# Optimization experiments

Measured on AMD Instinct MI355X. Metric: run time of the kernel, lower is better.

Reference implementation:

```python
import jax, jax.numpy as jnp
import numpy as np

B, T, D, H = 8, 1024, 512, 8
HD = D // H  # per-head hidden = embed_dim // n_head = 64
EPS = 1e-5


def setup_inputs() -> dict:
    key = jax.random.key(0)
    ks = jax.random.split(key, 8)
    x = jax.random.normal(ks[0], (B, T, D), dtype=jnp.float32)
    sc = 1.0 / np.sqrt(D)
    Wq = jax.random.normal(ks[1], (D, H * HD), dtype=jnp.float32) * sc
    Wk = jax.random.normal(ks[2], (D, H * HD), dtype=jnp.float32) * sc
    Wp = jax.random.normal(ks[3], (H * HD, D), dtype=jnp.float32) * sc
    bq = jnp.zeros((H * HD,), jnp.float32)
    bk = jnp.zeros((H * HD,), jnp.float32)
    bp = jnp.zeros((D,), jnp.float32)
    w_mlp = jax.random.normal(ks[4], (2 * HD,), dtype=jnp.float32) * 0.1
    ln_g = jnp.ones((D,), jnp.float32)
    ln_b = jnp.zeros((D,), jnp.float32)
    return {"x": x, "Wq": Wq, "bq": bq, "Wk": Wk, "bk": bk,
            "Wp": Wp, "bp": bp, "w_mlp": w_mlp, "ln_g": ln_g, "ln_b": ln_b}


def reference(x, Wq, bq, Wk, bk, Wp, bp, w_mlp, ln_g, ln_b):
    b, t, d = x.shape
    h, hd = H, HD
    # q/k projections, split into heads: [B,T,H,hd]
    qx = (x @ Wq + bq).reshape(b, t, h, hd)
    kx = (x @ Wk + bk).reshape(b, t, h, hd)
    # MLP score: tanh(concat(k_j, q_i) . w) == tanh(k_j.w[:hd] + q_i.w[hd:])
    k_s = jnp.einsum('bkhd,d->bkh', kx, w_mlp[:hd])   # [B,K,H]
    q_s = jnp.einsum('bqhd,d->bqh', qx, w_mlp[hd:])   # [B,Q,H]
    score = jnp.tanh(q_s[:, :, None, :] + k_s[:, None, :, :])  # [B,Q,K,H]
    attn = jax.nn.softmax(score, axis=2)  # softmax over k_len
    # values are the key projection kx (bmm(score, kx) in original)
    out = jnp.einsum('bqkh,bkhd->bqhd', attn, kx).reshape(b, t, h * hd)
    out = out @ Wp + bp  # output projection (dropout is identity at eval)
    # residual + LayerNorm
    y = x + out
    mu = jnp.mean(y, axis=-1, keepdims=True)
    var = jnp.var(y, axis=-1, keepdims=True)
    yn = (y - mu) * jax.lax.rsqrt(var + EPS)
    return yn * ln_g + ln_b
```

## Files before the change

kernel.cpp:

```cpp
#include <hip/hip_runtime.h>
#include <cstddef>

#define TT 1024
#define DDIM 512
#define HH 8
#define NND 128
#define NS 68

typedef __attribute__((ext_vector_type(8))) short bfrag;
typedef __attribute__((ext_vector_type(4))) float facc;

#define SC2   2.8853900817779268f
#define L2E   1.4426950408889634f

static __device__ __forceinline__ unsigned bfrne(float f) {
    unsigned u = __float_as_uint(f);
    return (u + 0x7fffu + ((u >> 16) & 1u)) >> 16;
}
static __device__ __forceinline__ unsigned pack2rne(float a, float b) {
    return bfrne(a) | (bfrne(b) << 16);
}
static __device__ __forceinline__ unsigned pack2hu(float a, float b) {
    return ((__float_as_uint(a) + 0x8000u) >> 16) |
           ((__float_as_uint(b) + 0x8000u) & 0xffff0000u);
}
static __device__ __forceinline__ void gl2lds16(const void* g, void* l) {
    __builtin_amdgcn_global_load_lds(
        (const __attribute__((address_space(1))) unsigned int*)g,
        (__attribute__((address_space(3))) unsigned int*)l, 16, 0, 0);
}
static __device__ __forceinline__ float wt(float t) {
    float r = __builtin_amdgcn_rcpf(t + 1.f);
    return __builtin_amdgcn_exp2f(fmaf(r, -2.f * L2E, L2E));
}

__global__ __launch_bounds__(256) void prepare_kernel(
    const float* __restrict__ x, const float* __restrict__ Wk,
    const float* __restrict__ Wp, const float* __restrict__ Wq,
    const float* __restrict__ bq, const float* __restrict__ wm,
    unsigned short* __restrict__ xb, unsigned short* __restrict__ WkT,
    unsigned short* __restrict__ WpT, unsigned short* __restrict__ vq2b,
    float* __restrict__ qsb2)
{
    const int bx = blockIdx.x, tid = threadIdx.x;
    if (bx < 2048) {
        const int lane = tid & 63, wave = tid >> 6;
        const int row = bx * 4 + wave;
        const float4* xr = (const float4*)(x + (size_t)row * DDIM);
        float4 x0 = xr[lane * 2], x1 = xr[lane * 2 + 1];
        uint4 st;
        st.x = pack2rne(x0.x, x0.y); st.y = pack2rne(x0.z, x0.w);
        st.z = pack2rne(x1.x, x1.y); st.w = pack2rne(x1.z, x1.w);
        int p = lane ^ (row & 7);
        *(uint4*)(xb + (size_t)row * DDIM + p * 8) = st;
    } else if (bx < 2176) {
        int idx = bx - 2048;
        const float* src = (idx & 64) ? Wp : Wk;
        unsigned short* dst = (idx & 64) ? WpT : WkT;
        idx &= 63;
        const int n0 = (idx & 7) * 64, k0 = (idx >> 3) * 64;
        __shared__ float sT[64][65];
        #pragma unroll
        for (int it = 0; it < 4; ++it) {
            int task = it * 256 + tid;
            int kr = task >> 4, c4 = (task & 15) * 4;
            float4 v = *(const float4*)(src + (size_t)(k0 + kr) * DDIM + n0 + c4);
            sT[kr][c4] = v.x; sT[kr][c4 + 1] = v.y; sT[kr][c4 + 2] = v.z; sT[kr][c4 + 3] = v.w;
        }
        __syncthreads();
        #pragma unroll
        for (int it = 0; it < 2; ++it) {
            int task = it * 256 + tid;
            int n = task >> 3, kg = task & 7;
            unsigned u[4];
            #pragma unroll
            for (int jj = 0; jj < 4; ++jj)
                u[jj] = pack2rne(sT[kg * 8 + jj * 2][n], sT[kg * 8 + jj * 2 + 1][n]);
            int p = ((k0 >> 3) + kg) ^ (n & 7);
            uint4 st; st.x = u[0]; st.y = u[1]; st.z = u[2]; st.w = u[3];
            *(uint4*)(dst + (size_t)(n0 + n) * DDIM + p * 8) = st;
        }
    } else {
        int idx = (bx - 2176) * 256 + tid;
        int h = idx >> 9, d = idx & 511;
        float s = 0.f;
        #pragma unroll 8
        for (int j = 0; j < 64; ++j)
            s = fmaf(Wq[(size_t)d * DDIM + h * 64 + j], wm[64 + j], s);
        vq2b[h * DDIM + d] = (unsigned short)bfrne(s * SC2);
        if (idx < HH) {
            float sb = 0.f;
            for (int j = 0; j < 64; ++j)
                sb = fmaf(bq[idx * 64 + j], wm[64 + j], sb);
            qsb2[idx] = sb * SC2;
        }
    }
}

__global__ __launch_bounds__(256) void gemm1_kernel(
    const unsigned short* __restrict__ A, const unsigned short* __restrict__ B,
    const float* __restrict__ bias, unsigned short* __restrict__ kxTg,
    float* __restrict__ ks2, const float* __restrict__ wm,
    const unsigned short* __restrict__ vq2b, const float* __restrict__ qsb2,
    float* __restrict__ qs2)
{
    __shared__ __align__(16) unsigned short smem[50176];
    unsigned short* svq = smem + 49152;
    const int tid = threadIdx.x, lane = tid & 63, wave = tid >> 6;
    const int l15 = lane & 15, quad = lane >> 4;
    const int wr = wave >> 1, wc = wave & 1;
    const int row0 = blockIdx.x * 128, colpair = blockIdx.y;
    const int h = colpair * 2 + wc, n0 = colpair * 128;

    const float qsbh = qsb2[h];
    float bvv[4], wmv[4];
    #pragma unroll
    for (int nt = 0; nt < 4; ++nt) {
        bvv[nt] = bias[h * 64 + nt * 16 + l15];
        wmv[nt] = wm[nt * 16 + l15] * SC2;
    }

    facc acc[4][4]; facc accq[4];
    #pragma unroll
    for (int i = 0; i < 4; ++i) {
        #pragma unroll
        for (int j = 0; j < 4; ++j) { acc[i][j][0]=0.f; acc[i][j][1]=0.f; acc[i][j][2]=0.f; acc[i][j][3]=0.f; }
        accq[i][0]=0.f; accq[i][1]=0.f; accq[i][2]=0.f; accq[i][3]=0.f;
    }

    if (tid < 128)
        gl2lds16(vq2b + colpair * 1024 + tid * 8, &svq[tid * 8]);

    auto stage = [&](int sel, int k0) {
        unsigned short* dA = smem + sel * 16384;
        unsigned short* dB = dA + 8192;
        #pragma unroll
        for (int it = 0; it < 4; ++it) {
            int g = it * 256 + tid;
            int r = g >> 3, kg = g & 7;
            gl2lds16(A + (size_t)(row0 + r) * 512 + k0 + kg * 8, &dA[g * 8]);
            gl2lds16(B + (size_t)(n0 + r) * 512 + k0 + kg * 8, &dB[g * 8]);
        }
    };

    stage(0, 0);
    stage(1, 64);
    #pragma unroll
    for (int kt = 0; kt < 8; ++kt) {
        const int sel = kt % 3;
        if (kt < 6) {
            stage((kt + 2) % 3, (kt + 2) * 64);
            asm volatile("s_waitcnt vmcnt(16)" ::: "memory");
        } else if (kt == 6) {
            asm volatile("s_waitcnt vmcnt(8)" ::: "memory");
        } else {
            asm volatile("s_waitcnt vmcnt(0)" ::: "memory");
        }
        __builtin_amdgcn_s_barrier();
        __builtin_amdgcn_sched_barrier(0);
        const unsigned short* sA = smem + sel * 16384;
        const unsigned short* sB = sA + 8192;
        #pragma unroll
        for (int ks_ = 0; ks_ < 2; ++ks_) {
            int slot = (ks_ * 4 + quad) ^ (l15 & 7);
            bfrag a[4], b[4];
            #pragma unroll
            for (int i = 0; i < 4; ++i) {
                a[i] = *(const bfrag*)&sA[(wr * 64 + i * 16 + l15) * 64 + slot * 8];
                b[i] = *(const bfrag*)&sB[(wc * 64 + i * 16 + l15) * 64 + slot * 8];
            }
            bfrag bvq = *(const bfrag*)&svq[wc * 512 + kt * 64 + ks_ * 32 + quad * 8];
            #pragma unroll
            for (int i = 0; i < 4; ++i) {
                #pragma unroll
                for (int nt = 0; nt < 4; ++nt)
                    acc[i][nt] = __builtin_amdgcn_mfma_f32_16x16x32_bf16(a[i], b[nt], acc[i][nt], 0, 0, 0);
                accq[i] = __builtin_amdgcn_mfma_f32_16x16x32_bf16(a[i], bvq, accq[i], 0, 0, 0);
            }
        }
        __builtin_amdgcn_s_barrier();
        __builtin_amdgcn_sched_barrier(0);
    }
    asm volatile("" ::: "memory");

    const int bb = row0 >> 10, t0 = row0 & 1023;
    float part[4][4];
    #pragma unroll
    for (int i = 0; i < 4; ++i)
        #pragma unroll
        for (int r = 0; r < 4; ++r) part[i][r] = 0.f;

    unsigned short* eT = smem + wc * 8704;
    #pragma unroll
    for (int i = 0; i < 4; ++i) {
        int tr = wr * 64 + i * 16 + quad * 4;
        #pragma unroll
        for (int nt = 0; nt < 4; ++nt) {
            int d = nt * 16 + l15;
            float v0 = acc[i][nt][0] + bvv[nt], v1 = acc[i][nt][1] + bvv[nt];
            float v2 = acc[i][nt][2] + bvv[nt], v3 = acc[i][nt][3] + bvv[nt];
            part[i][0] = fmaf(wmv[nt], v0, part[i][0]);
            part[i][1] = fmaf(wmv[nt], v1, part[i][1]);
            part[i][2] = fmaf(wmv[nt], v2, part[i][2]);
            part[i][3] = fmaf(wmv[nt], v3, part[i][3]);
            *(unsigned*)&eT[d * 136 + tr]     = pack2rne(v0, v1);
            *(unsigned*)&eT[d * 136 + tr + 2] = pack2rne(v2, v3);
        }
    }
    #pragma unroll
    for (int i = 0; i < 4; ++i)
        #pragma unroll
        for (int r = 0; r < 4; ++r) {
            float p = part[i][r];
            p += __shfl_xor(p, 1); p += __shfl_xor(p, 2);
            p += __shfl_xor(p, 4); p += __shfl_xor(p, 8);
            if (l15 == 0) {
                size_t o = (size_t)(bb * HH + h) * TT + t0 + wr * 64 + i * 16 + quad * 4 + r;
                ks2[o] = p;
                qs2[o] = accq[i][r] + qsbh;
            }
        }
    __syncthreads();
    #pragma unroll
    for (int it = 0; it < 8; ++it) {
        int task = it * 256 + tid;
        int hh = task >> 10, rem = task & 1023;
        int col = rem >> 4, seg = rem & 15;
        uint4 v = *(const uint4*)&smem[hh * 8704 + col * 136 + seg * 8];
        int hg = colpair * 2 + hh;
        int g = (t0 >> 3) + seg;
        int p = g ^ (col & 7);
        *(uint4*)(kxTg + ((size_t)(bb * HH + hg) * 64 + col) * TT + p * 8) = v;
    }
}

__global__ __launch_bounds__(256) void attn_kernel(
    const unsigned short* __restrict__ kxTg, const float* __restrict__ qs2,
    const float* __restrict__ ks2, unsigned short* __restrict__ attb)
{
    __shared__ __align__(16) unsigned short kxT[3 * 16384];
    __shared__ float tks[1024];
    __shared__ float redl[8];
    __shared__ __align__(16) float nodes[NND * NS];
    const int bh = blockIdx.x, thalf = blockIdx.y;
    const int b = bh >> 3, h = bh & 7;
    const int tid = threadIdx.x, lane = tid & 63, wave = tid >> 6;
    const int l15 = lane & 15, quad = lane >> 4;
    const unsigned short* kxbase = kxTg + (size_t)bh * 64 * TT;

    auto stage = [&](int sel, int ck) {
        unsigned short* dst = kxT + sel * 16384;
        #pragma unroll
        for (int it = 0; it < 8; ++it) {
            int g = it * 256 + tid;
            int d = g >> 5, j = g & 31;
            gl2lds16(kxbase + (size_t)d * TT + ck * 256 + j * 8, &dst[g * 8]);
        }
    };

    float4 ks4 = ((const float4*)(ks2 + (size_t)bh * TT))[tid];
    float4 q4  = ((const float4*)(qs2 + (size_t)bh * TT))[tid];
    stage(0, 0);
    stage(1, 1);
    float4 t4;
    t4.x = __builtin_amdgcn_exp2f(ks4.x);
    t4.y = __builtin_amdgcn_exp2f(ks4.y);
    t4.z = __builtin_amdgcn_exp2f(ks4.z);
    t4.w = __builtin_amdgcn_exp2f(ks4.w);
    ((float4*)tks)[tid] = t4;
    float mn = fminf(fminf(q4.x, q4.y), fminf(q4.z, q4.w));
    float mx = fmaxf(fmaxf(q4.x, q4.y), fmaxf(q4.z, q4.w));
    #pragma unroll
    for (int off = 32; off > 0; off >>= 1) {
        mn = fminf(mn, __shfl_xor(mn, off));
        mx = fmaxf(mx, __shfl_xor(mx, off));
    }
    if (lane == 0) { redl[wave] = mn; redl[4 + wave] = mx; }
    asm volatile("s_waitcnt lgkmcnt(0)" ::: "memory");
    __builtin_amdgcn_s_barrier();
    __builtin_amdgcn_sched_barrier(0);
    const float mnv = fminf(fminf(redl[0], redl[1]), fminf(redl[2], redl[3]));
    const float mxv = fmaxf(fmaxf(redl[4], redl[5]), fmaxf(redl[6], redl[7]));
    const float h2v = (mxv - mnv) * (1.f / 127.f);
    const float inv127v = 127.f / fmaxf(mxv - mnv, 1e-12f);
    const float zA = mnv + (wave * 16 + l15) * h2v;
    const float zB = zA + 64.f * h2v;
    const float tzA = __builtin_amdgcn_exp2f(zA);
    const float tzB = __builtin_amdgcn_exp2f(zB);

    facc acc[2][4]; facc accZ[2];
    #pragma unroll
    for (int g = 0; g < 2; ++g) {
        #pragma unroll
        for (int i = 0; i < 4; ++i) { acc[g][i][0]=0.f; acc[g][i][1]=0.f; acc[g][i][2]=0.f; acc[g][i][3]=0.f; }
        accZ[g][0]=0.f; accZ[g][1]=0.f; accZ[g][2]=0.f; accZ[g][3]=0.f;
    }
    bfrag ones;
    #pragma unroll
    for (int j = 0; j < 8; ++j) ones[j] = (short)0x3F80;

    #pragma unroll
    for (int ck = 0; ck < 4; ++ck) {
        const int sel = ck % 3;
        if (ck < 2) {
            stage((ck + 2) % 3, ck + 2);
            asm volatile("s_waitcnt vmcnt(16)" ::: "memory");
        } else if (ck == 2) {
            asm volatile("s_waitcnt vmcnt(8)" ::: "memory");
        } else {
            asm volatile("s_waitcnt vmcnt(0)" ::: "memory");
        }
        __builtin_amdgcn_s_barrier();
        __builtin_amdgcn_sched_barrier(0);
        const unsigned short* kx = kxT + sel * 16384;
        #pragma unroll
        for (int kst = 0; kst < 8; ++kst) {
            const float* kvp = &tks[ck * 256 + kst * 32 + quad * 8];
            float4 kv0 = *(const float4*)kvp;
            float4 kv1 = *(const float4*)(kvp + 4);
            int slot = (kst * 4 + quad) ^ (l15 & 7);
            bfrag bf_[4];
            #pragma unroll
            for (int dt = 0; dt < 4; ++dt)
                bf_[dt] = *(const bfrag*)&kx[(dt * 16 + l15) * 256 + slot * 8];
            #pragma unroll
            for (int g = 0; g < 2; ++g) {
                float tz = g ? tzB : tzA;
                union { unsigned u[4]; bfrag f; } afu;
                afu.u[0] = pack2hu(wt(tz * kv0.x), wt(tz * kv0.y));
                afu.u[1] = pack2hu(wt(tz * kv0.z), wt(tz * kv0.w));
                afu.u[2] = pack2hu(wt(tz * kv1.x), wt(tz * kv1.y));
                afu.u[3] = pack2hu(wt(tz * kv1.z), wt(tz * kv1.w));
                #pragma unroll
                for (int dt = 0; dt < 4; ++dt)
                    acc[g][dt] = __builtin_amdgcn_mfma_f32_16x16x32_bf16(afu.f, bf_[dt], acc[g][dt], 0, 0, 0);
                accZ[g] = __builtin_amdgcn_mfma_f32_16x16x32_bf16(afu.f, ones, accZ[g], 0, 0, 0);
            }
        }
        __builtin_amdgcn_s_barrier();
        __builtin_amdgcn_sched_barrier(0);
    }
    asm volatile("" ::: "memory");
    #pragma unroll
    for (int g = 0; g < 2; ++g) {
        #pragma unroll
        for (int r = 0; r < 4; ++r) {
            int node = g * 64 + wave * 16 + quad * 4 + r;
            #pragma unroll
            for (int dt = 0; dt < 4; ++dt)
                nodes[node * NS + dt * 16 + l15] = acc[g][dt][r];
            if (l15 == 0) nodes[node * NS + 64] = accZ[g][r];
        }
    }
    __syncthreads();

    const float* qsp = qs2 + (size_t)bh * TT;
    #pragma unroll 2
    for (int it = 0; it < 32; ++it) {
        int task = it * 256 + tid;
        int t = thalf * 512 + (task >> 4), dp = task & 15;
        float qv = qsp[t];
        float u = (qv - mnv) * inv127v;
        int i = (int)floorf(u) - 1;
        i = i < 0 ? 0 : (i > NND - 4 ? NND - 4 : i);
        float s = u - (float)i;
        float s1 = s - 1.f, s2 = s - 2.f, s3 = s - 3.f;
        float w0 = -s1 * s2 * s3 * (1.f / 6.f);
        float w1 = s * s2 * s3 * 0.5f;
        float w2 = -s * s1 * s3 * 0.5f;
        float w3 = s * s1 * s2 * (1.f / 6.f);
        const float* base = &nodes[i * NS];
        float4 v0 = *(const float4*)(base + 4 * dp);
        float4 v1 = *(const float4*)(base + NS + 4 * dp);
        float4 v2 = *(const float4*)(base + 2 * NS + 4 * dp);
        float4 v3 = *(const float4*)(base + 3 * NS + 4 * dp);
        float zz = w0 * base[64] + w1 * base[NS + 64] + w2 * base[2 * NS + 64] + w3 * base[3 * NS + 64];
        float ox = w0 * v0.x + w1 * v1.x + w2 * v2.x + w3 * v3.x;
        float oy = w0 * v0.y + w1 * v1.y + w2 * v2.y + w3 * v3.y;
        float oz = w0 * v0.z + w1 * v1.z + w2 * v2.z + w3 * v3.z;
        float ow = w0 * v0.w + w1 * v1.w + w2 * v2.w + w3 * v3.w;
        float rz = __builtin_amdgcn_rcpf(zz);
        uint2 st;
        st.x = pack2rne(ox * rz, oy * rz);
        st.y = pack2rne(oz * rz, ow * rz);
        int row = b * TT + t;
        int col = h * 64 + 4 * dp;
        int p = (col >> 3) ^ (row & 7);
        *(uint2*)&attb[(size_t)row * DDIM + p * 8 + (col & 7)] = st;
    }
}

__global__ __launch_bounds__(256) void gemm2_kernel(
    const unsigned short* __restrict__ A, const unsigned short* __restrict__ B,
    const float* __restrict__ bias, unsigned short* __restrict__ yb)
{
    __shared__ __align__(16) unsigned short smem[49152];
    const int tid = threadIdx.x, lane = tid & 63, wave = tid >> 6;
    const int l15 = lane & 15, quad = lane >> 4;
    const int wr = wave >> 1, wc = wave & 1;
    const int row0 = blockIdx.x * 128, col0 = blockIdx.y * 128;

    float bvv[4];
    #pragma unroll
    for (int nt = 0; nt < 4; ++nt) bvv[nt] = bias[col0 + wc * 64 + nt * 16 + l15];

    facc acc[4][4];
    #pragma unroll
    for (int i = 0; i < 4; ++i)
        #pragma unroll
        for (int j = 0; j < 4; ++j) { acc[i][j][0]=0.f; acc[i][j][1]=0.f; acc[i][j][2]=0.f; acc[i][j][3]=0.f; }

    auto stage = [&](int sel, int k0) {
        unsigned short* dA = smem + sel * 16384;
        unsigned short* dB = dA + 8192;
        #pragma unroll
        for (int it = 0; it < 4; ++it) {
            int g = it * 256 + tid;
            int r = g >> 3, kg = g & 7;
            gl2lds16(A + (size_t)(row0 + r) * 512 + k0 + kg * 8, &dA[g * 8]);
            gl2lds16(B + (size_t)(col0 + r) * 512 + k0 + kg * 8, &dB[g * 8]);
        }
    };

    stage(0, 0);
    stage(1, 64);
    #pragma unroll
    for (int kt = 0; kt < 8; ++kt) {
        const int sel = kt % 3;
        if (kt < 6) {
            stage((kt + 2) % 3, (kt + 2) * 64);
            asm volatile("s_waitcnt vmcnt(16)" ::: "memory");
        } else if (kt == 6) {
            asm volatile("s_waitcnt vmcnt(8)" ::: "memory");
        } else {
            asm volatile("s_waitcnt vmcnt(0)" ::: "memory");
        }
        __builtin_amdgcn_s_barrier();
        __builtin_amdgcn_sched_barrier(0);
        const unsigned short* sA = smem + sel * 16384;
        const unsigned short* sB = sA + 8192;
        #pragma unroll
        for (int ks_ = 0; ks_ < 2; ++ks_) {
            int slot = (ks_ * 4 + quad) ^ (l15 & 7);
            bfrag a[4], b[4];
            #pragma unroll
            for (int i = 0; i < 4; ++i) {
                a[i] = *(const bfrag*)&sA[(wr * 64 + i * 16 + l15) * 64 + slot * 8];
                b[i] = *(const bfrag*)&sB[(wc * 64 + i * 16 + l15) * 64 + slot * 8];
            }
            #pragma unroll
            for (int i = 0; i < 4; ++i)
                #pragma unroll
                for (int nt = 0; nt < 4; ++nt)
                    acc[i][nt] = __builtin_amdgcn_mfma_f32_16x16x32_bf16(a[i], b[nt], acc[i][nt], 0, 0, 0);
        }
        __builtin_amdgcn_s_barrier();
        __builtin_amdgcn_sched_barrier(0);
    }
    asm volatile("" ::: "memory");

    unsigned short* yT = smem;
    #pragma unroll
    for (int i = 0; i < 4; ++i) {
        #pragma unroll
        for (int nt = 0; nt < 4; ++nt) {
            int col = wc * 64 + nt * 16 + l15;
            #pragma unroll
            for (int r = 0; r < 4; ++r) {
                int row = wr * 64 + i * 16 + quad * 4 + r;
                yT[row * 136 + col] = (unsigned short)bfrne(acc[i][nt][r] + bvv[nt]);
            }
        }
    }
    __syncthreads();
    #pragma unroll
    for (int it = 0; it < 8; ++it) {
        int task = it * 256 + tid;
        int row = task >> 4, seg = task & 15;
        uint4 v = *(const uint4*)&yT[row * 136 + seg * 8];
        *(uint4*)(yb + (size_t)(row0 + row) * DDIM + col0 + seg * 8) = v;
    }
}

__global__ __launch_bounds__(256) void ln_kernel(
    const unsigned short* __restrict__ yb, const unsigned short* __restrict__ xb,
    const float* __restrict__ g, const float* __restrict__ bet,
    float* __restrict__ out)
{
    const int tid = threadIdx.x, lane = tid & 63, wave = tid >> 6;
    const int row = blockIdx.x * 4 + wave;
    uint4 pv = *(const uint4*)(yb + (size_t)row * DDIM + lane * 8);
    int pgr = lane ^ (row & 7);
    uint4 xv = *(const uint4*)(xb + (size_t)row * DDIM + pgr * 8);
    float y[8];
    const unsigned* pu = (const unsigned*)&pv;
    const unsigned* xu = (const unsigned*)&xv;
    #pragma unroll
    for (int j = 0; j < 4; ++j) {
        y[2*j]   = __uint_as_float(pu[j] << 16)        + __uint_as_float(xu[j] << 16);
        y[2*j+1] = __uint_as_float(pu[j] & 0xffff0000u) + __uint_as_float(xu[j] & 0xffff0000u);
    }
    float s = 0.f, s2 = 0.f;
    #pragma unroll
    for (int i = 0; i < 8; ++i) { s += y[i]; s2 = fmaf(y[i], y[i], s2); }
    #pragma unroll
    for (int off = 32; off > 0; off >>= 1) {
        s += __shfl_xor(s, off);
        s2 += __shfl_xor(s2, off);
    }
    float mu = s * (1.f / 512.f);
    float var = s2 * (1.f / 512.f) - mu * mu;
    float inv = rsqrtf(var + 1e-5f);
    const float4* gp = (const float4*)(g + lane * 8);
    const float4* bp = (const float4*)(bet + lane * 8);
    float4 g0 = gp[0], g1 = gp[1], b0 = bp[0], b1 = bp[1];
    float4 o0, o1;
    o0.x = (y[0] - mu) * inv * g0.x + b0.x; o0.y = (y[1] - mu) * inv * g0.y + b0.y;
    o0.z = (y[2] - mu) * inv * g0.z + b0.z; o0.w = (y[3] - mu) * inv * g0.w + b0.w;
    o1.x = (y[4] - mu) * inv * g1.x + b1.x; o1.y = (y[5] - mu) * inv * g1.y + b1.y;
    o1.z = (y[6] - mu) * inv * g1.z + b1.z; o1.w = (y[7] - mu) * inv * g1.w + b1.w;
    float4* op = (float4*)(out + (size_t)row * DDIM);
    op[lane * 2] = o0; op[lane * 2 + 1] = o1;
}

extern "C" void kernel_launch(void* const* d_in, const int* in_sizes, int n_in,
                              void* d_out, int out_size, void* d_ws, size_t ws_size,
                              hipStream_t stream)
{
    const float* x    = (const float*)d_in[0];
    const float* Wq   = (const float*)d_in[1];
    const float* bq   = (const float*)d_in[2];
    const float* Wk   = (const float*)d_in[3];
    const float* bk   = (const float*)d_in[4];
    const float* Wp   = (const float*)d_in[5];
    const float* bp   = (const float*)d_in[6];
    const float* wm   = (const float*)d_in[7];
    const float* ln_g = (const float*)d_in[8];
    const float* ln_b = (const float*)d_in[9];
    float* out = (float*)d_out;

    float* ws = (float*)d_ws;
    float*          qsb2 = ws;
    unsigned short* vq2b = (unsigned short*)(ws + 64);
    unsigned short* WkT  = (unsigned short*)(ws + 2112);
    unsigned short* WpT  = (unsigned short*)(ws + 133184);
    unsigned short* xb   = (unsigned short*)(ws + 264256);
    unsigned short* kxTg = (unsigned short*)(ws + 2361408);
    float*          qs2  = ws + 4458560;
    float*          ks2  = ws + 4524096;
    unsigned short* attb = (unsigned short*)(ws + 4589632);
    unsigned short* yb   = (unsigned short*)(ws + 6686784);

    prepare_kernel<<<2192, 256, 0, stream>>>(x, Wk, Wp, Wq, bq, wm,
                                             xb, WkT, WpT, vq2b, qsb2);
    gemm1_kernel<<<dim3(64, 4), 256, 0, stream>>>(xb, WkT, bk, kxTg, ks2, wm,
                                                  vq2b, qsb2, qs2);
    attn_kernel<<<dim3(64, 2), 256, 0, stream>>>(kxTg, qs2, ks2, attb);
    gemm2_kernel<<<dim3(64, 4), 256, 0, stream>>>(attb, WpT, bp, yb);
    ln_kernel<<<2048, 256, 0, stream>>>(yb, xb, ln_g, ln_b, out);
}
```

Before: 138.4 us.

## Split attention into K-chunked node kernel and interpolation kernel; wave-reduce Wq·w

The single attention kernel previously streamed all 1024 keys per (batch, head) with only 128 blocks. It is now split into a nodes kernel that processes one 256-key chunk per block, writing partial node sums to global memory, and an interp kernel that sums the four partials and interpolates over 256-query slices. This raises the block count to fill more CUs, at the cost of an extra launch and a global round trip for the partials. The prepare kernel's Wq·w reduction also changes from one thread per output to one wave per output using shuffle reductions, which gives coalesced loads but needs more blocks.

```diff
diff --git a/kernel.cpp b/kernel.cpp
--- a/kernel.cpp
+++ b/kernel.cpp
@@ -43,8 +43,8 @@
     float* __restrict__ qsb2)
 {
     const int bx = blockIdx.x, tid = threadIdx.x;
+    const int lane = tid & 63, wave = tid >> 6;
     if (bx < 2048) {
-        const int lane = tid & 63, wave = tid >> 6;
         const int row = bx * 4 + wave;
         const float4* xr = (const float4*)(x + (size_t)row * DDIM);
         float4 x0 = xr[lane * 2], x1 = xr[lane * 2 + 1];
@@ -81,18 +81,17 @@
             *(uint4*)(dst + (size_t)(n0 + n) * DDIM + p * 8) = st;
         }
     } else {
-        int idx = (bx - 2176) * 256 + tid;
+        int idx = (bx - 2176) * 4 + wave;
         int h = idx >> 9, d = idx & 511;
-        float s = 0.f;
-        #pragma unroll 8
-        for (int j = 0; j < 64; ++j)
-            s = fmaf(Wq[(size_t)d * DDIM + h * 64 + j], wm[64 + j], s);
-        vq2b[h * DDIM + d] = (unsigned short)bfrne(s * SC2);
-        if (idx < HH) {
+        float v = Wq[(size_t)d * DDIM + h * 64 + lane] * wm[64 + lane];
+        #pragma unroll
+        for (int off = 32; off > 0; off >>= 1) v += __shfl_xor(v, off);
+        if (lane == 0) vq2b[h * DDIM + d] = (unsigned short)bfrne(v * SC2);
+        if (bx == 2176 && tid < HH) {
             float sb = 0.f;
             for (int j = 0; j < 64; ++j)
-                sb = fmaf(bq[idx * 64 + j], wm[64 + j], sb);
-            qsb2[idx] = sb * SC2;
+                sb = fmaf(bq[tid * 64 + j], wm[64 + j], sb);
+            qsb2[tid] = sb * SC2;
         }
     }
 }
@@ -234,40 +233,27 @@
     }
 }
 
-__global__ __launch_bounds__(256) void attn_kernel(
+__global__ __launch_bounds__(256) void nodes_kernel(
     const unsigned short* __restrict__ kxTg, const float* __restrict__ qs2,
-    const float* __restrict__ ks2, unsigned short* __restrict__ attb)
-{
-    __shared__ __align__(16) unsigned short kxT[3 * 16384];
-    __shared__ float tks[1024];
+    const float* __restrict__ ks2, float* __restrict__ npart)
+{
+    __shared__ __align__(16) unsigned short kxT[16384];
+    __shared__ float tks[256];
     __shared__ float redl[8];
-    __shared__ __align__(16) float nodes[NND * NS];
-    const int bh = blockIdx.x, thalf = blockIdx.y;
-    const int b = bh >> 3, h = bh & 7;
+    const int bh = blockIdx.x, kq = blockIdx.y;
     const int tid = threadIdx.x, lane = tid & 63, wave = tid >> 6;
     const int l15 = lane & 15, quad = lane >> 4;
     const unsigned short* kxbase = kxTg + (size_t)bh * 64 * TT;
 
-    auto stage = [&](int sel, int ck) {
-        unsigned short* dst = kxT + sel * 16384;
-        #pragma unroll
-        for (int it = 0; it < 8; ++it) {
-            int g = it * 256 + tid;
-            int d = g >> 5, j = g & 31;
-            gl2lds16(kxbase + (size_t)d * TT + ck * 256 + j * 8, &dst[g * 8]);
-        }
-    };
-
-    float4 ks4 = ((const float4*)(ks2 + (size_t)bh * TT))[tid];
-    float4 q4  = ((const float4*)(qs2 + (size_t)bh * TT))[tid];
-    stage(0, 0);
-    stage(1, 1);
-    float4 t4;
-    t4.x = __builtin_amdgcn_exp2f(ks4.x);
-    t4.y = __builtin_amdgcn_exp2f(ks4.y);
-    t4.z = __builtin_amdgcn_exp2f(ks4.z);
-    t4.w = __builtin_amdgcn_exp2f(ks4.w);
-    ((float4*)tks)[tid] = t4;
+    #pragma unroll
+    for (int it = 0; it < 8; ++it) {
+        int g = it * 256 + tid;
+        int d = g >> 5, j = g & 31;
+        gl2lds16(kxbase + (size_t)d * TT + kq * 256 + j * 8, &kxT[g * 8]);
+    }
+    float ksv = ks2[(size_t)bh * TT + kq * 256 + tid];
+    float4 q4 = ((const float4*)(qs2 + (size_t)bh * TT))[tid];
+    tks[tid] = __builtin_amdgcn_exp2f(ksv);
     float mn = fminf(fminf(q4.x, q4.y), fminf(q4.z, q4.w));
     float mx = fmaxf(fmaxf(q4.x, q4.y), fmaxf(q4.z, q4.w));
     #pragma unroll
@@ -276,13 +262,10 @@
         mx = fmaxf(mx, __shfl_xor(mx, off));
     }
     if (lane == 0) { redl[wave] = mn; redl[4 + wave] = mx; }
-    asm volatile("s_waitcnt lgkmcnt(0)" ::: "memory");
-    __builtin_amdgcn_s_barrier();
-    __builtin_amdgcn_sched_barrier(0);
+    __syncthreads();
     const float mnv = fminf(fminf(redl[0], redl[1]), fminf(redl[2], redl[3]));
     const float mxv = fmaxf(fmaxf(redl[4], redl[5]), fmaxf(redl[6], redl[7]));
     const float h2v = (mxv - mnv) * (1.f / 127.f);
-    const float inv127v = 127.f / fmaxf(mxv - mnv, 1e-12f);
     const float zA = mnv + (wave * 16 + l15) * h2v;
     const float zB = zA + 64.f * h2v;
     const float tzA = __builtin_amdgcn_exp2f(zA);
@@ -300,65 +283,90 @@
     for (int j = 0; j < 8; ++j) ones[j] = (short)0x3F80;
 
     #pragma unroll
-    for (int ck = 0; ck < 4; ++ck) {
-        const int sel = ck % 3;
-        if (ck < 2) {
-            stage((ck + 2) % 3, ck + 2);
-            asm volatile("s_waitcnt vmcnt(16)" ::: "memory");
-        } else if (ck == 2) {
-            asm volatile("s_waitcnt vmcnt(8)" ::: "memory");
-        } else {
-            asm volatile("s_waitcnt vmcnt(0)" ::: "memory");
-        }
-        __builtin_amdgcn_s_barrier();
-        __builtin_amdgcn_sched_barrier(0);
-        const unsigned short* kx = kxT + sel * 16384;
-        #pragma unroll
-        for (int kst = 0; kst < 8; ++kst) {
-            const float* kvp = &tks[ck * 256 + kst * 32 + quad * 8];
-            float4 kv0 = *(const float4*)kvp;
-            float4 kv1 = *(const float4*)(kvp + 4);
-            int slot = (kst * 4 + quad) ^ (l15 & 7);
-            bfrag bf_[4];
+    for (int kst = 0; kst < 8; ++kst) {
+        const float* kvp = &tks[kst * 32 + quad * 8];
+        float4 kv0 = *(const float4*)kvp;
+        float4 kv1 = *(const float4*)(kvp + 4);
+        int slot = (kst * 4 + quad) ^ (l15 & 7);
+        bfrag bf_[4];
+        #pragma unroll
+        for (int dt = 0; dt < 4; ++dt)
+            bf_[dt] = *(const bfrag*)&kxT[(dt * 16 + l15) * 256 + slot * 8];
+        #pragma unroll
+        for (int g = 0; g < 2; ++g) {
+            float tz = g ? tzB : tzA;
+            union { unsigned u[4]; bfrag f; } afu;
+            afu.u[0] = pack2hu(wt(tz * kv0.x), wt(tz * kv0.y));
+            afu.u[1] = pack2hu(wt(tz * kv0.z), wt(tz * kv0.w));
+            afu.u[2] = pack2hu(wt(tz * kv1.x), wt(tz * kv1.y));
+            afu.u[3] = pack2hu(wt(tz * kv1.z), wt(tz * kv1.w));
             #pragma unroll
             for (int dt = 0; dt < 4; ++dt)
-                bf_[dt] = *(const bfrag*)&kx[(dt * 16 + l15) * 256 + slot * 8];
-            #pragma unroll
-            for (int g = 0; g < 2; ++g) {
-                float tz = g ? tzB : tzA;
-                union { unsigned u[4]; bfrag f; } afu;
-                afu.u[0] = pack2hu(wt(tz * kv0.x), wt(tz * kv0.y));
-                afu.u[1] = pack2hu(wt(tz * kv0.z), wt(tz * kv0.w));
-                afu.u[2] = pack2hu(wt(tz * kv1.x), wt(tz * kv1.y));
-                afu.u[3] = pack2hu(wt(tz * kv1.z), wt(tz * kv1.w));
-                #pragma unroll
-                for (int dt = 0; dt < 4; ++dt)
-                    acc[g][dt] = __builtin_amdgcn_mfma_f32_16x16x32_bf16(afu.f, bf_[dt], acc[g][dt], 0, 0, 0);
-                accZ[g] = __builtin_amdgcn_mfma_f32_16x16x32_bf16(afu.f, ones, accZ[g], 0, 0, 0);
-            }
-        }
-        __builtin_amdgcn_s_barrier();
-        __builtin_amdgcn_sched_barrier(0);
-    }
-    asm volatile("" ::: "memory");
-    #pragma unroll
-    for (int g = 0; g < 2; ++g) {
+                acc[g][dt] = __builtin_amdgcn_mfma_f32_16x16x32_bf16(afu.f, bf_[dt], acc[g][dt], 0, 0, 0);
+            accZ[g] = __builtin_amdgcn_mfma_f32_16x16x32_bf16(afu.f, ones, accZ[g], 0, 0, 0);
+        }
+    }
+    float* dst = npart + (size_t)(bh * 4 + kq) * (NND * NS);
+    #pragma unroll
+    for (int g = 0; g < 2; ++g)
         #pragma unroll
         for (int r = 0; r < 4; ++r) {
             int node = g * 64 + wave * 16 + quad * 4 + r;
             #pragma unroll
             for (int dt = 0; dt < 4; ++dt)
-                nodes[node * NS + dt * 16 + l15] = acc[g][dt][r];
-            if (l15 == 0) nodes[node * NS + 64] = accZ[g][r];
+                dst[node * NS + dt * 16 + l15] = acc[g][dt][r];
+            if (l15 == 0) dst[node * NS + 64] = accZ[g][r];
+        }
+}
+
+__global__ __launch_bounds__(256) void interp_kernel(
+    const float* __restrict__ npart, const float* __restrict__ qs2,
+    unsigned short* __restrict__ attb)
+{
+    __shared__ __align__(16) float nodes[NND * NS];
+    __shared__ float redl[8];
+    const int bh = blockIdx.x, tq = blockIdx.y;
+    const int b = bh >> 3, h = bh & 7;
+    const int tid = threadIdx.x, lane = tid & 63, wave = tid >> 6;
+
+    float4 q4 = ((const float4*)(qs2 + (size_t)bh * TT))[tid];
+    float mn = fminf(fminf(q4.x, q4.y), fminf(q4.z, q4.w));
+    float mx = fmaxf(fmaxf(q4.x, q4.y), fmaxf(q4.z, q4.w));
+    #pragma unroll
+    for (int off = 32; off > 0; off >>= 1) {
+        mn = fminf(mn, __shfl_xor(mn, off));
+        mx = fmaxf(mx, __shfl_xor(mx, off));
+    }
+    if (lane == 0) { redl[wave] = mn; redl[4 + wave] = mx; }
+    __syncthreads();
+    const float mnv = fminf(fminf(redl[0], redl[1]), fminf(redl[2], redl[3]));
+    const float mxv = fmaxf(fmaxf(redl[4], redl[5]), fmaxf(redl[6], redl[7]));
+    const float inv127v = 127.f / fmaxf(mxv - mnv, 1e-12f);
+
+    const float4* p0 = (const float4*)(npart + (size_t)(bh * 4 + 0) * (NND * NS));
+    const float4* p1 = (const float4*)(npart + (size_t)(bh * 4 + 1) * (NND * NS));
+    const float4* p2 = (const float4*)(npart + (size_t)(bh * 4 + 2) * (NND * NS));
+    const float4* p3 = (const float4*)(npart + (size_t)(bh * 4 + 3) * (NND * NS));
+    #pragma unroll
+    for (int it = 0; it < 9; ++it) {
+        int g = it * 256 + tid;
+        if (g < (NND * NS) / 4) {
+            float4 a = p0[g], bb4 = p1[g], c = p2[g], d = p3[g];
+            float4 s;
+            s.x = a.x + bb4.x + c.x + d.x;
+            s.y = a.y + bb4.y + c.y + d.y;
+            s.z = a.z + bb4.z + c.z + d.z;
+            s.w = a.w + bb4.w + c.w + d.w;
+            ((float4*)nodes)[g] = s;
         }
     }
     __syncthreads();
 
     const float* qsp = qs2 + (size_t)bh * TT;
     #pragma unroll 2
-    for (int it = 0; it < 32; ++it) {
+    for (int it = 0; it < 16; ++it) {
         int task = it * 256 + tid;
-        int t = thalf * 512 + (task >> 4), dp = task & 15;
+        int t = tq * 256 + (task >> 4), dp = task & 15;
         float qv = qsp[t];
         float u = (qv - mnv) * inv127v;
         int i = (int)floorf(u) - 1;
@@ -550,12 +558,14 @@
     float*          ks2  = ws + 4524096;
     unsigned short* attb = (unsigned short*)(ws + 4589632);
     unsigned short* yb   = (unsigned short*)(ws + 6686784);
-
-    prepare_kernel<<<2192, 256, 0, stream>>>(x, Wk, Wp, Wq, bq, wm,
+    float*          npart = ws + 8783936;
+
+    prepare_kernel<<<3200, 256, 0, stream>>>(x, Wk, Wp, Wq, bq, wm,
                                              xb, WkT, WpT, vq2b, qsb2);
     gemm1_kernel<<<dim3(64, 4), 256, 0, stream>>>(xb, WkT, bk, kxTg, ks2, wm,
                                                   vq2b, qsb2, qs2);
-    attn_kernel<<<dim3(64, 2), 256, 0, stream>>>(kxTg, qs2, ks2, attb);
+    nodes_kernel<<<dim3(64, 4), 256, 0, stream>>>(kxTg, qs2, ks2, npart);
+    interp_kernel<<<dim3(64, 4), 256, 0, stream>>>(npart, qs2, attb);
     gemm2_kernel<<<dim3(64, 4), 256, 0, stream>>>(attb, WpT, bp, yb);
     ln_kernel<<<2048, 256, 0, stream>>>(yb, xb, ln_g, ln_b, out);
 }
```

Result: faster. 131.3 us (-5.1%).
